# Kernel optimization log

Measured on AMD Instinct MI355X. Metric: run time of the kernel, lower is better.

The kernel has to match this reference:

```python
import jax, jax.numpy as jnp
import numpy as np

B, N, C, K = 64, 32768, 2, 10   # batch, num predictions, num classes, padded GT slots (build_target default N=10)
VL = 1.0e6                      # 'very_large' sentinel from torch code
EPS = 1e-08
W_LOC = W_CLASS = W_CONF = 1.0


def setup_inputs() -> dict:
    key = jax.random.key(0)
    k1, k2, k3, k4, k5, k6, k7 = jax.random.split(key, 7)
    p_start = jax.random.normal(k1, (B, N), dtype=jnp.float32)
    p_end = jax.random.normal(k2, (B, N), dtype=jnp.float32)
    p_class_logits = jax.random.normal(k3, (B, N, C), dtype=jnp.float32)
    p_conf_logits = jax.random.normal(k4, (B, N), dtype=jnp.float32)
    # GT intervals in [0,1] (compared against sigmoid(pred)); class channel in {0,1}
    fs = jax.random.uniform(k5, (B, K), dtype=jnp.float32)
    fe = jnp.clip(fs + 0.2 * jax.random.uniform(k6, (B, K), dtype=jnp.float32), 0.0, 1.0)
    cls = jax.random.randint(k7, (B, K), 0, C).astype(jnp.float32)
    gt_boxes = jnp.stack([fs, fe, cls], axis=-1)  # (B, K, 3)
    return {'p_start': p_start, 'p_end': p_end, 'p_class_logits': p_class_logits,
            'p_conf_logits': p_conf_logits, 'gt_boxes': gt_boxes}


def _build_target(gt_boxes):
    fs, fe, cls = gt_boxes[..., 0], gt_boxes[..., 1], gt_boxes[..., 2]
    presence = (~(jnp.isnan(fs) | jnp.isnan(fe) | jnp.isnan(cls))).astype(jnp.float32)
    fs = jnp.nan_to_num(fs)
    fe = jnp.nan_to_num(fe)
    cls = jnp.nan_to_num(cls)
    onehot = jax.nn.one_hot(jnp.clip(cls.astype(jnp.int32), 0, C - 1), C, dtype=jnp.float32)
    return fs, fe, onehot, presence


def _match_and_losses(cost, ps, pe, pcl, pconf, fs, fe, onehot):
    # cost: (K, N); greedy one-to-one argmin matching with row/col masking.
    Kp, Np = cost.shape

    def step(c, _):
        flat = c.reshape(-1)
        idx = jnp.argmin(flat)
        val = flat[idx]
        row, col = idx // Np, idx % Np
        valid = val < VL / 2
        c = c.at[row, :].set(VL).at[:, col].set(VL)
        return c, (row, col, valid)

    _, (rows, cols, valids) = jax.lax.scan(step, jax.lax.stop_gradient(cost), None, length=Kp)
    vm = valids.astype(jnp.float32)  # (K,)

    sel_s = jax.nn.sigmoid(ps[cols])
    sel_e = jax.nn.sigmoid(pe[cols])
    gs, ge = fs[rows], fe[rows]
    loc = (sel_s - gs) ** 2 + (sel_e - ge) ** 2

    logits = pcl[cols]          # (K, C)
    y = onehot[rows]            # (K, C)
    bce = (y * jax.nn.softplus(-logits) + (1.0 - y) * jax.nn.softplus(logits)).sum(-1)

    # IoU target is computed from .item() values in torch -> constant (no grad)
    ss, se = jax.lax.stop_gradient(sel_s), jax.lax.stop_gradient(sel_e)
    gss, gse = jax.lax.stop_gradient(gs), jax.lax.stop_gradient(ge)
    a1, b1 = jnp.minimum(ss, se), jnp.maximum(ss, se)
    a2, b2 = jnp.minimum(gss, gse), jnp.maximum(gss, gse)
    inter = jnp.maximum(0.0, jnp.minimum(b1, b2) - jnp.maximum(a1, a2))
    union = jnp.maximum(EPS, jnp.maximum(b1, b2) - jnp.minimum(a1, a2))
    iou = inter / union
    conf = (jax.nn.sigmoid(pconf[cols]) - iou) ** 2

    return (loc * vm).sum(), (bce * vm).sum(), (conf * vm).sum(), vm.sum()


def reference(p_start, p_end, p_class_logits, p_conf_logits, gt_boxes):
    fs, fe, onehot, presence = _build_target(gt_boxes)  # (B,K), (B,K), (B,K,C), (B,K)
    ps_sig = jax.nn.sigmoid(p_start)
    pe_sig = jax.nn.sigmoid(p_end)
    # loc MSE cost: (B, K, N)
    loc = (ps_sig[:, None, :] - fs[:, :, None]) ** 2 + (pe_sig[:, None, :] - fe[:, :, None]) ** 2
    # class L2 cost without materializing (B,K,N,C): |a-b|^2 = |a|^2 - 2 a.b + |b|^2
    sc = jax.nn.sigmoid(p_class_logits)  # (B, N, C)
    class_l2 = ((sc ** 2).sum(-1)[:, None, :]
                - 2.0 * jnp.einsum('bnc,bkc->bkn', sc, onehot)
                + (onehot ** 2).sum(-1)[:, :, None])
    cost = loc + class_l2
    # invalid (absent) GT rows get sentinel cost so greedy skips them
    cost = jnp.where(presence[:, :, None] > 0, cost, VL)

    loc_s, cls_s, conf_s, m = jax.vmap(_match_and_losses)(
        cost, p_start, p_end, p_class_logits, p_conf_logits, fs, fe, onehot)

    total_m = m.sum()
    denom = total_m + EPS
    total = (W_LOC * loc_s.sum() + W_CLASS * cls_s.sum() + W_CONF * conf_s.sum()) / denom
    return jnp.where(total_m > 0, total, 0.0)
```

## Files before the change

### kernel.cpp

```cpp
#include <hip/hip_runtime.h>
#include <cfloat>
#include <cmath>

#define BB 64
#define NN 32768
#define CC 2
#define KK 10
#define S_SL 32
#define SLICE (NN / S_SL)
#define VLARGE 1.0e6
#define KEY_MAX 0xFFFFFFFFFFFFFFFFull
#define BND_MARGIN 1.0e-4

__device__ __forceinline__ float fsig(float x) {
    return __fdividef(1.0f, 1.0f + __expf(-x));
}
__device__ __forceinline__ double dsig(float x) { return 1.0 / (1.0 + exp(-(double)x)); }
__device__ __forceinline__ double dsoftplus(double x) {
    return fmax(x, 0.0) + log1p(exp(-fabs(x)));
}
__device__ __forceinline__ unsigned long long packkey(float v, int c) {
    return ((unsigned long long)__float_as_uint(v) << 32) | (unsigned int)c;
}
__device__ __forceinline__ void merge2(unsigned long long& a1, unsigned long long& a2,
                                       unsigned long long b1, unsigned long long b2) {
    unsigned long long lo = a1 < b1 ? a1 : b1;
    unsigned long long hi = a1 < b1 ? b1 : a1;
    unsigned long long mb = a2 < b2 ? a2 : b2;
    a2 = hi < mb ? hi : mb;
    a1 = lo;
}
__device__ __forceinline__ float costf(float xs, float xe, float xc0, float xc1,
                                       float ffs, float ffe, int cls, int pres) {
    if (!pres) return (float)VLARGE;
    const float s = fsig(xs), e = fsig(xe), q0 = fsig(xc0), q1 = fsig(xc1);
    const float t0 = q0 - 1.0f, t1 = q1 - 1.0f;
    const float cp = (cls == 0) ? fmaf(t0, t0, q1 * q1) : fmaf(t1, t1, q0 * q0);
    const float d0 = s - ffs, d1 = e - ffe;
    return fmaf(d0, d0, fmaf(d1, d1, cp));
}
__device__ __forceinline__ double eval64(const float* ps, const float* pe, const float* pc,
                                         double fs, double fe, int cls, int pres, int col) {
    if (!pres) return VLARGE;
    const double s  = dsig(ps[col]);
    const double e  = dsig(pe[col]);
    const double q0 = dsig(pc[2 * col]);
    const double q1 = dsig(pc[2 * col + 1]);
    const double d0 = s - fs, d1 = e - fe;
    const double sc = (cls == 0) ? q0 : q1;
    return d0 * d0 + d1 * d1 + (q0 * q0 + q1 * q1 - 2.0 * sc + 1.0);
}

__global__ __launch_bounds__(64)
void scan_kernel(const float* __restrict__ p_start, const float* __restrict__ p_end,
                 const float* __restrict__ p_cls, const float* __restrict__ gt,
                 ulonglong2* __restrict__ cand) {
    const int sl = blockIdx.x, b = blockIdx.y, j = threadIdx.x;
    const float2* ps2 = (const float2*)(p_start + (size_t)b * NN);
    const float2* pe2 = (const float2*)(p_end   + (size_t)b * NN);
    const float4* pc4 = (const float4*)(p_cls   + (size_t)b * NN * CC);

    float rfs[KK], rfe[KK]; int rcl[KK], rpres[KK];
    #pragma unroll
    for (int k = 0; k < KK; k++) {
        float f0 = gt[((size_t)b * KK + k) * 3 + 0];
        float f1 = gt[((size_t)b * KK + k) * 3 + 1];
        float f2 = gt[((size_t)b * KK + k) * 3 + 2];
        int pres = !(isnan(f0) || isnan(f1) || isnan(f2));
        if (isnan(f0)) f0 = 0.0f;
        if (isnan(f1)) f1 = 0.0f;
        if (isnan(f2)) f2 = 0.0f;
        int ci = (int)f2; ci = ci < 0 ? 0 : (ci > CC - 1 ? CC - 1 : ci);
        rfs[k] = f0; rfe[k] = f1; rcl[k] = ci; rpres[k] = pres;
    }

    float v1[KK], v2[KK]; int c1[KK], c2[KK];
    #pragma unroll
    for (int k = 0; k < KK; k++) { v1[k] = FLT_MAX; v2[k] = FLT_MAX; c1[k] = 0x7fffffff; c2[k] = 0x7fffffff; }

    const int base = sl * SLICE;
    #pragma unroll
    for (int it = 0; it < SLICE / 128; it++) {
        const int pidx = (base >> 1) + it * 64 + j;
        const float2 sv = ps2[pidx];
        const float2 ev = pe2[pidx];
        const float4 cv = pc4[pidx];
        #pragma unroll
        for (int h = 0; h < 2; h++) {
            const int n = 2 * pidx + h;
            const float s  = fsig(h ? sv.y : sv.x);
            const float e  = fsig(h ? ev.y : ev.x);
            const float q0 = fsig(h ? cv.z : cv.x);
            const float q1 = fsig(h ? cv.w : cv.y);
            const float t0 = q0 - 1.0f, t1 = q1 - 1.0f;
            const float cp0 = fmaf(t0, t0, q1 * q1);
            const float cp1 = fmaf(t1, t1, q0 * q0);
            #pragma unroll
            for (int k = 0; k < KK; k++) {
                const float d0 = s - rfs[k], d1 = e - rfe[k];
                float cost = fmaf(d0, d0, fmaf(d1, d1, (rcl[k] == 0) ? cp0 : cp1));
                if (!rpres[k]) cost = (float)VLARGE;
                const bool lt1 = cost < v1[k], lt2 = cost < v2[k];
                v2[k] = lt2 ? (lt1 ? v1[k] : cost) : v2[k];
                c2[k] = lt2 ? (lt1 ? c1[k] : n)    : c2[k];
                v1[k] = lt1 ? cost : v1[k];
                c1[k] = lt1 ? n    : c1[k];
            }
        }
    }

    unsigned long long k1[KK], k2[KK];
    #pragma unroll
    for (int k = 0; k < KK; k++) { k1[k] = packkey(v1[k], c1[k]); k2[k] = packkey(v2[k], c2[k]); }
    #pragma unroll
    for (int off = 1; off < 64; off <<= 1) {
        #pragma unroll
        for (int k = 0; k < KK; k++) {
            unsigned long long o1 = __shfl_xor(k1[k], off, 64);
            unsigned long long o2 = __shfl_xor(k2[k], off, 64);
            merge2(k1[k], k2[k], o1, o2);
        }
    }
    if (j == 0) {
        #pragma unroll
        for (int k = 0; k < KK; k++) {
            ulonglong2 pk; pk.x = k1[k]; pk.y = k2[k];
            cand[((size_t)b * S_SL + sl) * KK + k] = pk;
        }
    }
}

__global__ __launch_bounds__(64)
void match_kernel(const float* __restrict__ p_start, const float* __restrict__ p_end,
                  const float* __restrict__ p_cls, const float* __restrict__ p_conf,
                  const float* __restrict__ gt, const ulonglong2* __restrict__ cand,
                  double* __restrict__ partials) {
    const int b = blockIdx.x, j = threadIdx.x;
    const int s_my = j >> 1;
    const float* ps  = p_start + (size_t)b * NN;
    const float* pe  = p_end   + (size_t)b * NN;
    const float* pc  = p_cls   + (size_t)b * NN * CC;
    const float* pcf = p_conf  + (size_t)b * NN;

    __shared__ double gfs[KK], gfe[KK];
    __shared__ int    gcls[KK], gpres[KK];
    __shared__ int    s_prow[KK], s_pcol[KK], s_pvalid[KK], s_cons[KK];

    float myf0 = 0.0f, myf1 = 0.0f; int myci = 0, mypres = 1;
    if (j < KK) {
        float f0 = gt[((size_t)b * KK + j) * 3 + 0];
        float f1 = gt[((size_t)b * KK + j) * 3 + 1];
        float f2 = gt[((size_t)b * KK + j) * 3 + 2];
        mypres = !(isnan(f0) || isnan(f1) || isnan(f2));
        if (isnan(f0)) f0 = 0.0f;
        if (isnan(f1)) f1 = 0.0f;
        if (isnan(f2)) f2 = 0.0f;
        int ci = (int)f2; ci = ci < 0 ? 0 : (ci > CC - 1 ? CC - 1 : ci);
        myf0 = f0; myf1 = f1; myci = ci;
        gfs[j] = (double)f0; gfe[j] = (double)f1; gcls[j] = ci; gpres[j] = mypres;
    }
    __syncthreads();

    double fsr[KK], fer[KK]; int clsr[KK], presr[KK];
    #pragma unroll
    for (int r = 0; r < KK; r++) {
        fsr[r]  = (double)__shfl(myf0, r, 64);
        fer[r]  = (double)__shfl(myf1, r, 64);
        clsr[r] = __shfl(myci, r, 64);
        presr[r] = __shfl(mypres, r, 64);
    }

    double val[KK]; int col[KK]; double bnd[KK]; int blive[KK];
    #pragma unroll
    for (int r = 0; r < KK; r++) {
        ulonglong2 pk = cand[((size_t)b * S_SL + s_my) * KK + r];
        unsigned long long key = (j & 1) ? pk.y : pk.x;
        const int c = (int)(unsigned int)(key & 0xffffffffull);
        col[r] = c;
        val[r] = eval64(ps, pe, pc, fsr[r], fer[r], clsr[r], presr[r], c);
    }
    #pragma unroll
    for (int r = 0; r < KK; r++) {
        bnd[r] = __shfl(val[r], j | 1, 64) - BND_MARGIN;
        blive[r] = 1;
    }

    unsigned act = (1u << KK) - 1;

    for (int step = 0; step < KK; step++) {
        double bv; int br, bc;
        while (true) {
            bv = DBL_MAX; br = 0; bc = -1;
            #pragma unroll
            for (int r = 0; r < KK; r++) {
                if (!((act >> r) & 1)) continue;
                const int pcold = __shfl(col[r], j ^ 1, 64);
                double ev = val[r]; int ec = col[r];
                const bool bothdead = (col[r] < 0) && (pcold < 0);
                if (((j & 1) == 0) && bothdead && blive[r]) { ev = bnd[r]; ec = -2 - s_my; }
                #pragma unroll
                for (int off = 1; off < 64; off <<= 1) {
                    double ov = __shfl_xor(ev, off, 64);
                    int    oc = __shfl_xor(ec, off, 64);
                    if (ov < ev || (ov == ev && oc < ec)) { ev = ov; ec = oc; }
                }
                if (ev < bv) { bv = ev; br = r; bc = ec; }
            }
            if (bc >= -1) break;

            const int ss  = -2 - bc;
            const float ffs = __shfl(myf0, br, 64), ffe = __shfl(myf1, br, 64);
            const int   cb  = __shfl(myci, br, 64);
            const int   pb  = __shfl(mypres, br, 64);
            unsigned long long r1 = KEY_MAX, r2 = KEY_MAX;
            const int cbase = ss * SLICE;
            #pragma unroll 4
            for (int t = j; t < SLICE; t += 64) {
                const int n = cbase + t;
                bool used = false;
                for (int u = 0; u < step; u++) if (s_cons[u] == n) used = true;
                const float cst = costf(ps[n], pe[n], pc[2 * n], pc[2 * n + 1], ffs, ffe, cb, pb);
                const unsigned long long kk = used ? KEY_MAX : packkey(cst, n);
                if (kk < r2) { if (kk < r1) { r2 = r1; r1 = kk; } else r2 = kk; }
            }
            #pragma unroll
            for (int off = 1; off < 64; off <<= 1) {
                unsigned long long o1 = __shfl_xor(r1, off, 64);
                unsigned long long o2 = __shfl_xor(r2, off, 64);
                merge2(r1, r2, o1, o2);
            }
            const int cA = (int)(unsigned int)(r1 & 0xffffffffull);
            const int cB = (int)(unsigned int)(r2 & 0xffffffffull);
            const double dfs = (double)ffs, dfe = (double)ffe;
            const double vA = (r1 == KEY_MAX) ? DBL_MAX : eval64(ps, pe, pc, dfs, dfe, cb, pb, cA);
            const double vB = (r2 == KEY_MAX) ? DBL_MAX : eval64(ps, pe, pc, dfs, dfe, cb, pb, cB);
            #pragma unroll
            for (int rr = 0; rr < KK; rr++) {
                if (rr != br) continue;
                if (s_my == ss) {
                    if ((j & 1) == 0) { val[rr] = vA; col[rr] = (r1 == KEY_MAX) ? -1 : cA; }
                    else              { val[rr] = vB; col[rr] = (r2 == KEY_MAX) ? -1 : cB; }
                    blive[rr] = (r2 != KEY_MAX) ? 1 : 0;
                    bnd[rr]   = (r2 != KEY_MAX) ? (vB - BND_MARGIN) : DBL_MAX;
                }
            }
        }

        act &= ~(1u << br);
        if (j == 0) {
            s_prow[step] = br; s_pcol[step] = bc;
            s_pvalid[step] = (bv < VLARGE * 0.5) && (bc >= 0);
            s_cons[step] = bc;
        }
        __syncthreads();
        if (bc >= 0) {
            #pragma unroll
            for (int r = 0; r < KK; r++)
                if (col[r] == bc) { val[r] = DBL_MAX; col[r] = -1; }
        }
    }

    double loss = 0.0, m = 0.0;
    if (j < KK && s_pvalid[j]) {
        const int r = s_prow[j], cidx = s_pcol[j];
        const double ss = dsig(ps[cidx]);
        const double se = dsig(pe[cidx]);
        const double gs = gfs[r], ge = gfe[r];
        const double d0 = ss - gs, d1 = se - ge;
        double acc = d0 * d0 + d1 * d1;

        const double l0 = (double)pc[2 * cidx];
        const double l1 = (double)pc[2 * cidx + 1];
        const double y0 = (gcls[r] == 0) ? 1.0 : 0.0;
        const double y1 = 1.0 - y0;
        acc += y0 * dsoftplus(-l0) + (1.0 - y0) * dsoftplus(l0)
             + y1 * dsoftplus(-l1) + (1.0 - y1) * dsoftplus(l1);

        const double a1 = fmin(ss, se), b1 = fmax(ss, se);
        const double a2 = fmin(gs, ge), b2 = fmax(gs, ge);
        const double inter = fmax(0.0, fmin(b1, b2) - fmax(a1, a2));
        const double uni   = fmax(1e-8, fmax(b1, b2) - fmin(a1, a2));
        const double iou   = inter / uni;
        const double dcf   = dsig(pcf[cidx]) - iou;
        acc += dcf * dcf;
        loss = acc; m = 1.0;
    }
    #pragma unroll
    for (int off = 1; off < 64; off <<= 1) {
        loss += __shfl_xor(loss, off, 64);
        m    += __shfl_xor(m, off, 64);
    }
    if (j == 0) { partials[b * 2 + 0] = loss; partials[b * 2 + 1] = m; }
}

__global__ void finalize_kernel(const double* __restrict__ partials,
                                float* __restrict__ out, int out_size) {
    const int t = threadIdx.x;
    for (int i = t; i < out_size; i += 64) out[i] = 0.0f;
    double s = partials[t * 2 + 0];
    double m = partials[t * 2 + 1];
    for (int off = 32; off > 0; off >>= 1) {
        s += __shfl_down(s, off, 64);
        m += __shfl_down(m, off, 64);
    }
    if (t == 0) {
        const double total = s / (m + 1e-8);
        out[0] = (float)(m > 0.0 ? total : 0.0);
    }
}

extern "C" void kernel_launch(void* const* d_in, const int* in_sizes, int n_in,
                              void* d_out, int out_size, void* d_ws, size_t ws_size,
                              hipStream_t stream) {
    const float* p_start = (const float*)d_in[0];
    const float* p_end   = (const float*)d_in[1];
    const float* p_cls   = (const float*)d_in[2];
    const float* p_conf  = (const float*)d_in[3];
    const float* gt      = (const float*)d_in[4];

    ulonglong2* cand     = (ulonglong2*)d_ws;
    double*     partials = (double*)((char*)d_ws + (size_t)BB * S_SL * KK * sizeof(ulonglong2));

    scan_kernel<<<dim3(S_SL, BB), 64, 0, stream>>>(p_start, p_end, p_cls, gt, cand);
    match_kernel<<<BB, 64, 0, stream>>>(p_start, p_end, p_cls, p_conf, gt, cand, partials);
    finalize_kernel<<<1, 64, 0, stream>>>(partials, (float*)d_out, out_size);
}
```

Before: 173.3 us.

## Parallelize candidate evaluation and collapse per-row reductions in greedy matcher

The match kernel now launches 256 threads per batch. All of them evaluate the 640 initial candidate costs in double precision into shared memory, and then a single wave runs the greedy selection. Each selection iteration does a per-lane min over the ten rows followed by one wave-wide reduction on (value, row, col), replacing ten separate row reductions. Consumed-column state and the per-step results move into registers, which removes the shared-memory bookkeeping and the per-step block barriers. The trade-off is a new rescan rule: any lane with a consumed column now turns its stale value into a bound, which may trigger more slice rescans than the old rule that required both lanes of a pair to be dead.

```diff
diff --git a/kernel.cpp b/kernel.cpp
--- a/kernel.cpp
+++ b/kernel.cpp
@@ -8,6 +8,7 @@
 #define KK 10
 #define S_SL 32
 #define SLICE (NN / S_SL)
+#define TPM 256
 #define VLARGE 1.0e6
 #define KEY_MAX 0xFFFFFFFFFFFFFFFFull
 #define BND_MARGIN 1.0e-4
@@ -130,139 +131,126 @@
     }
 }
 
-__global__ __launch_bounds__(64)
+__global__ __launch_bounds__(TPM)
 void match_kernel(const float* __restrict__ p_start, const float* __restrict__ p_end,
                   const float* __restrict__ p_cls, const float* __restrict__ p_conf,
                   const float* __restrict__ gt, const ulonglong2* __restrict__ cand,
                   double* __restrict__ partials) {
-    const int b = blockIdx.x, j = threadIdx.x;
-    const int s_my = j >> 1;
+    const int b = blockIdx.x, tid = threadIdx.x;
+    const int j = tid & 63, wv = tid >> 6;
     const float* ps  = p_start + (size_t)b * NN;
     const float* pe  = p_end   + (size_t)b * NN;
     const float* pc  = p_cls   + (size_t)b * NN * CC;
     const float* pcf = p_conf  + (size_t)b * NN;
 
+    __shared__ double l_cost[KK][64];
+    __shared__ int    l_col[KK][64];
     __shared__ double gfs[KK], gfe[KK];
     __shared__ int    gcls[KK], gpres[KK];
-    __shared__ int    s_prow[KK], s_pcol[KK], s_pvalid[KK], s_cons[KK];
-
-    float myf0 = 0.0f, myf1 = 0.0f; int myci = 0, mypres = 1;
-    if (j < KK) {
-        float f0 = gt[((size_t)b * KK + j) * 3 + 0];
-        float f1 = gt[((size_t)b * KK + j) * 3 + 1];
-        float f2 = gt[((size_t)b * KK + j) * 3 + 2];
-        mypres = !(isnan(f0) || isnan(f1) || isnan(f2));
+
+    if (tid < KK) {
+        float f0 = gt[((size_t)b * KK + tid) * 3 + 0];
+        float f1 = gt[((size_t)b * KK + tid) * 3 + 1];
+        float f2 = gt[((size_t)b * KK + tid) * 3 + 2];
+        int pres = !(isnan(f0) || isnan(f1) || isnan(f2));
         if (isnan(f0)) f0 = 0.0f;
         if (isnan(f1)) f1 = 0.0f;
         if (isnan(f2)) f2 = 0.0f;
         int ci = (int)f2; ci = ci < 0 ? 0 : (ci > CC - 1 ? CC - 1 : ci);
-        myf0 = f0; myf1 = f1; myci = ci;
-        gfs[j] = (double)f0; gfe[j] = (double)f1; gcls[j] = ci; gpres[j] = mypres;
+        gfs[tid] = (double)f0; gfe[tid] = (double)f1;
+        gcls[tid] = ci; gpres[tid] = pres;
     }
     __syncthreads();
 
-    double fsr[KK], fer[KK]; int clsr[KK], presr[KK];
-    #pragma unroll
-    for (int r = 0; r < KK; r++) {
-        fsr[r]  = (double)__shfl(myf0, r, 64);
-        fer[r]  = (double)__shfl(myf1, r, 64);
-        clsr[r] = __shfl(myci, r, 64);
-        presr[r] = __shfl(mypres, r, 64);
-    }
-
-    double val[KK]; int col[KK]; double bnd[KK]; int blive[KK];
-    #pragma unroll
-    for (int r = 0; r < KK; r++) {
-        ulonglong2 pk = cand[((size_t)b * S_SL + s_my) * KK + r];
-        unsigned long long key = (j & 1) ? pk.y : pk.x;
+    for (int idx = tid; idx < KK * 64; idx += TPM) {
+        const int r = idx >> 6, jj = idx & 63, sl = jj >> 1;
+        ulonglong2 pk = cand[((size_t)b * S_SL + sl) * KK + r];
+        const unsigned long long key = (jj & 1) ? pk.y : pk.x;
         const int c = (int)(unsigned int)(key & 0xffffffffull);
-        col[r] = c;
-        val[r] = eval64(ps, pe, pc, fsr[r], fer[r], clsr[r], presr[r], c);
-    }
-    #pragma unroll
-    for (int r = 0; r < KK; r++) {
-        bnd[r] = __shfl(val[r], j | 1, 64) - BND_MARGIN;
-        blive[r] = 1;
-    }
-
-    unsigned act = (1u << KK) - 1;
+        l_cost[r][jj] = eval64(ps, pe, pc, gfs[r], gfe[r], gcls[r], gpres[r], c);
+        l_col[r][jj]  = c;
+    }
+    __syncthreads();
+    if (wv != 0) return;
+
+    double val[KK]; int col[KK];
+    #pragma unroll
+    for (int r = 0; r < KK; r++) { val[r] = l_cost[r][j]; col[r] = l_col[r][j]; }
+
+    const int s_my = j >> 1;
+    int cons[KK], prow[KK], pcolv[KK], pvalid[KK];
+    #pragma unroll
+    for (int r = 0; r < KK; r++) cons[r] = -1;
 
     for (int step = 0; step < KK; step++) {
-        double bv; int br, bc;
-        while (true) {
-            bv = DBL_MAX; br = 0; bc = -1;
+        double bv = DBL_MAX; int brow = 0x7fffffff, bcol = 0x7fffffff;
+        for (int guard = 0; guard < 1024; guard++) {
+            double lv = DBL_MAX; int lr = 0x7fffffff, lc = 0x7fffffff;
             #pragma unroll
             for (int r = 0; r < KK; r++) {
-                if (!((act >> r) & 1)) continue;
-                const int pcold = __shfl(col[r], j ^ 1, 64);
-                double ev = val[r]; int ec = col[r];
-                const bool bothdead = (col[r] < 0) && (pcold < 0);
-                if (((j & 1) == 0) && bothdead && blive[r]) { ev = bnd[r]; ec = -2 - s_my; }
-                #pragma unroll
-                for (int off = 1; off < 64; off <<= 1) {
-                    double ov = __shfl_xor(ev, off, 64);
-                    int    oc = __shfl_xor(ec, off, 64);
-                    if (ov < ev || (ov == ev && oc < ec)) { ev = ov; ec = oc; }
+                double v = val[r]; int c = col[r];
+                if (c < 0) { v -= BND_MARGIN; c = -2 - s_my; }
+                if (v < lv || (v == lv && (r < lr || (r == lr && c < lc)))) { lv = v; lr = r; lc = c; }
+            }
+            #pragma unroll
+            for (int off = 1; off < 64; off <<= 1) {
+                const double ov = __shfl_xor(lv, off, 64);
+                const int   orr = __shfl_xor(lr, off, 64);
+                const int   oc  = __shfl_xor(lc, off, 64);
+                if (ov < lv || (ov == lv && (orr < lr || (orr == lr && oc < lc)))) {
+                    lv = ov; lr = orr; lc = oc;
                 }
-                if (ev < bv) { bv = ev; br = r; bc = ec; }
-            }
-            if (bc >= -1) break;
-
-            const int ss  = -2 - bc;
-            const float ffs = __shfl(myf0, br, 64), ffe = __shfl(myf1, br, 64);
-            const int   cb  = __shfl(myci, br, 64);
-            const int   pb  = __shfl(mypres, br, 64);
+            }
+            bv = lv; brow = lr; bcol = lc;
+            if (bcol >= 0 || bv == DBL_MAX) break;
+
+            const int ss  = -2 - bcol;
+            const float ffs = (float)gfs[brow], ffe = (float)gfe[brow];
+            const int   cb  = gcls[brow], pb = gpres[brow];
             unsigned long long r1 = KEY_MAX, r2 = KEY_MAX;
             const int cbase = ss * SLICE;
-            #pragma unroll 4
             for (int t = j; t < SLICE; t += 64) {
                 const int n = cbase + t;
                 bool used = false;
-                for (int u = 0; u < step; u++) if (s_cons[u] == n) used = true;
+                #pragma unroll
+                for (int u = 0; u < KK; u++) used |= (u < step) && (cons[u] == n);
                 const float cst = costf(ps[n], pe[n], pc[2 * n], pc[2 * n + 1], ffs, ffe, cb, pb);
                 const unsigned long long kk = used ? KEY_MAX : packkey(cst, n);
-                if (kk < r2) { if (kk < r1) { r2 = r1; r1 = kk; } else r2 = kk; }
+                if (kk < r2) { if (kk < r1) { r2 = r1; r1 = kk; } else { r2 = kk; } }
             }
             #pragma unroll
             for (int off = 1; off < 64; off <<= 1) {
-                unsigned long long o1 = __shfl_xor(r1, off, 64);
-                unsigned long long o2 = __shfl_xor(r2, off, 64);
+                const unsigned long long o1 = __shfl_xor(r1, off, 64);
+                const unsigned long long o2 = __shfl_xor(r2, off, 64);
                 merge2(r1, r2, o1, o2);
             }
             const int cA = (int)(unsigned int)(r1 & 0xffffffffull);
             const int cB = (int)(unsigned int)(r2 & 0xffffffffull);
-            const double dfs = (double)ffs, dfe = (double)ffe;
-            const double vA = (r1 == KEY_MAX) ? DBL_MAX : eval64(ps, pe, pc, dfs, dfe, cb, pb, cA);
-            const double vB = (r2 == KEY_MAX) ? DBL_MAX : eval64(ps, pe, pc, dfs, dfe, cb, pb, cB);
-            #pragma unroll
-            for (int rr = 0; rr < KK; rr++) {
-                if (rr != br) continue;
-                if (s_my == ss) {
-                    if ((j & 1) == 0) { val[rr] = vA; col[rr] = (r1 == KEY_MAX) ? -1 : cA; }
-                    else              { val[rr] = vB; col[rr] = (r2 == KEY_MAX) ? -1 : cB; }
-                    blive[rr] = (r2 != KEY_MAX) ? 1 : 0;
-                    bnd[rr]   = (r2 != KEY_MAX) ? (vB - BND_MARGIN) : DBL_MAX;
-                }
-            }
-        }
-
-        act &= ~(1u << br);
-        if (j == 0) {
-            s_prow[step] = br; s_pcol[step] = bc;
-            s_pvalid[step] = (bv < VLARGE * 0.5) && (bc >= 0);
-            s_cons[step] = bc;
-        }
-        __syncthreads();
-        if (bc >= 0) {
-            #pragma unroll
-            for (int r = 0; r < KK; r++)
-                if (col[r] == bc) { val[r] = DBL_MAX; col[r] = -1; }
+            const double vA = eval64(ps, pe, pc, gfs[brow], gfe[brow], cb, pb, cA);
+            const double vB = eval64(ps, pe, pc, gfs[brow], gfe[brow], cb, pb, cB);
+            #pragma unroll
+            for (int r = 0; r < KK; r++) {
+                if (r != brow) continue;
+                if (j == 2 * ss)     { val[r] = vA; col[r] = cA; }
+                if (j == 2 * ss + 1) { val[r] = vB; col[r] = cB; }
+            }
+        }
+
+        prow[step]   = brow;
+        pcolv[step]  = bcol;
+        pvalid[step] = (bv < VLARGE * 0.5) && (bcol >= 0) && (brow < KK);
+        cons[step]   = bcol;
+
+        #pragma unroll
+        for (int r = 0; r < KK; r++) {
+            if (r == brow) val[r] = DBL_MAX;
+            if (bcol >= 0 && col[r] == bcol) col[r] = -1;
         }
     }
 
     double loss = 0.0, m = 0.0;
-    if (j < KK && s_pvalid[j]) {
-        const int r = s_prow[j], cidx = s_pcol[j];
+    if (j < KK && pvalid[j]) {
+        const int r = prow[j], cidx = pcolv[j];
         const double ss = dsig(ps[cidx]);
         const double se = dsig(pe[cidx]);
         const double gs = gfs[r], ge = gfe[r];
@@ -322,6 +310,6 @@
     double*     partials = (double*)((char*)d_ws + (size_t)BB * S_SL * KK * sizeof(ulonglong2));
 
     scan_kernel<<<dim3(S_SL, BB), 64, 0, stream>>>(p_start, p_end, p_cls, gt, cand);
-    match_kernel<<<BB, 64, 0, stream>>>(p_start, p_end, p_cls, p_conf, gt, cand, partials);
+    match_kernel<<<BB, TPM, 0, stream>>>(p_start, p_end, p_cls, p_conf, gt, cand, partials);
     finalize_kernel<<<1, 64, 0, stream>>>(partials, (float*)d_out, out_size);
 }
```

Result: slower. 203.7 us (+17.5%).
